# Kernel tuning notes

Measured on AMD Instinct MI355X. Metric: run time of the kernel, lower is better.

Reference implementation:

```python
import jax, jax.numpy as jnp
import numpy as np

B, S, D, H = 2, 2048, 1024, 16
DEPTH = D // H


def setup_inputs() -> dict:
    key = jax.random.key(0)
    ks = jax.random.split(key, 13)
    std = 1.0 / np.sqrt(D)
    inp = {
        'q': jax.random.normal(ks[0], (B, S, D), jnp.float32),
        'k': jax.random.normal(ks[1], (B, S, D), jnp.float32),
        'v': jax.random.normal(ks[2], (B, S, D), jnp.float32),
        # padding-style mask broadcastable to [B,H,Sq,Sk]; 1 = masked
        'mask': (jax.random.uniform(ks[3], (B, 1, 1, S)) < 0.1).astype(jnp.float32),
        'wq_w': jax.random.uniform(ks[4], (D, D), jnp.float32, -std, std),
        'wq_b': jax.random.uniform(ks[5], (D,), jnp.float32, -std, std),
        'wk_w': jax.random.uniform(ks[6], (D, D), jnp.float32, -std, std),
        'wk_b': jax.random.uniform(ks[7], (D,), jnp.float32, -std, std),
        'wv_w': jax.random.uniform(ks[8], (D, D), jnp.float32, -std, std),
        'wv_b': jax.random.uniform(ks[9], (D,), jnp.float32, -std, std),
        'wo_w': jax.random.uniform(ks[10], (D, D), jnp.float32, -std, std),
        'wo_b': jax.random.uniform(ks[11], (D,), jnp.float32, -std, std),
    }
    return inp


def _split_heads(x):
    # [B,S,D] -> [B,H,S,depth]
    b, s, _ = x.shape
    return x.reshape(b, s, H, DEPTH).transpose(0, 2, 1, 3)


def reference(q, k, v, mask, wq_w, wq_b, wk_w, wk_b, wv_w, wv_b, wo_w, wo_b):
    qh = _split_heads(q @ wq_w.T + wq_b)
    kh = _split_heads(k @ wk_w.T + wk_b)
    vh = _split_heads(v @ wv_w.T + wv_b)
    scale = 1.0 / jnp.sqrt(jnp.float32(DEPTH))
    logits = jnp.einsum('bhqd,bhkd->bhqk', qh, kh) * scale  # [B,H,S,S]
    logits = logits + mask * (-1e9)
    weights = jax.nn.softmax(logits, axis=-1)
    attn = jnp.einsum('bhqk,bhkd->bhqd', weights, vh)
    concat = attn.transpose(0, 2, 1, 3).reshape(q.shape[0], -1, D)
    out = concat @ wo_w.T + wo_b
    return out, weights
```

## Files before the change

### kernel.cpp

```cpp
#include <hip/hip_runtime.h>
#include <stdint.h>
#include <stddef.h>

static constexpr int NB = 2;
static constexpr int SS = 2048;
static constexpr int DDim = 1024;
static constexpr int NH = 16;
static constexpr size_t BSD = (size_t)NB * SS * DDim;
static constexpr size_t DDn = (size_t)DDim * DDim;

typedef __attribute__((ext_vector_type(4))) float f32x4;
typedef __attribute__((ext_vector_type(8))) short bf16x8;

__device__ __forceinline__ short f2bf(float f) {
  union { float f; unsigned u; } v; v.f = f;
  unsigned r = v.u + 0x7FFFu + ((v.u >> 16) & 1u);
  return (short)(r >> 16);
}

__device__ __forceinline__ void gload_lds16(const void* src, void* dst) {
  __builtin_amdgcn_global_load_lds(
      (const __attribute__((address_space(1))) void*)src,
      (__attribute__((address_space(3))) void*)dst, 16, 0, 0);
}

__global__ void cvt_k(const float* __restrict__ in, short* __restrict__ out, int n8) {
  int i = blockIdx.x * 256 + threadIdx.x;
  if (i >= n8) return;
  const f32x4* p = (const f32x4*)in + (size_t)i * 2;
  f32x4 a = p[0], c = p[1];
  bf16x8 o;
  o[0] = f2bf(a[0]); o[1] = f2bf(a[1]); o[2] = f2bf(a[2]); o[3] = f2bf(a[3]);
  o[4] = f2bf(c[0]); o[5] = f2bf(c[1]); o[6] = f2bf(c[2]); o[7] = f2bf(c[3]);
  ((bf16x8*)out)[i] = o;
}

__device__ __forceinline__ void gemm_core(
    const short* __restrict__ A, const short* __restrict__ Bm,
    int rowA, int rowB, int ld, int nk,
    short* la, short* lb, int wid, int lane, f32x4 (&acc)[4][4]) {
  const int ar = lane & 15, ak = (lane >> 4) * 8;
  const int srow = lane >> 2, scol = (lane & 3) * 8;
  const int wr = wid >> 1, wc = wid & 1;
  for (int kt = 0; kt < nk; ++kt) {
    const int k0 = kt * 32;
#pragma unroll
    for (int c = 0; c < 2; ++c) {
      int chunk = c * 4 + wid;
      gload_lds16(A + (size_t)(rowA + chunk * 16 + srow) * ld + k0 + scol, la + chunk * 512);
      gload_lds16(Bm + (size_t)(rowB + chunk * 16 + srow) * ld + k0 + scol, lb + chunk * 512);
    }
    asm volatile("s_waitcnt vmcnt(0)" ::: "memory");
    __syncthreads();
    bf16x8 af[4], bfr[4];
#pragma unroll
    for (int m = 0; m < 4; ++m)
      af[m] = *(const bf16x8*)(la + (wr * 64 + m * 16 + ar) * 32 + ak);
#pragma unroll
    for (int n = 0; n < 4; ++n)
      bfr[n] = *(const bf16x8*)(lb + (wc * 64 + n * 16 + ar) * 32 + ak);
#pragma unroll
    for (int m = 0; m < 4; ++m)
#pragma unroll
      for (int n = 0; n < 4; ++n)
        acc[m][n] = __builtin_amdgcn_mfma_f32_16x16x32_bf16(af[m], bfr[n], acc[m][n], 0, 0, 0);
    __syncthreads();
  }
}

template <int MODE>
__global__ __launch_bounds__(256, 2) void gemm128(
    const short* __restrict__ A, const short* __restrict__ Bm,
    const float* __restrict__ bias, void* __restrict__ outp, int N, int ld, int nk) {
  __shared__ short la[128 * 32], lb[128 * 32];
  const int tid = threadIdx.x, wid = tid >> 6, lane = tid & 63;
  const int bM = blockIdx.y * 128, bN = blockIdx.x * 128;
  f32x4 acc[4][4];
#pragma unroll
  for (int m = 0; m < 4; ++m)
#pragma unroll
    for (int n = 0; n < 4; ++n) acc[m][n] = (f32x4){0.f, 0.f, 0.f, 0.f};
  gemm_core(A, Bm, bM, bN, ld, nk, la, lb, wid, lane, acc);
  const int wr = wid >> 1, wc = wid & 1;
#pragma unroll
  for (int m = 0; m < 4; ++m)
#pragma unroll
    for (int n = 0; n < 4; ++n)
#pragma unroll
      for (int r = 0; r < 4; ++r) {
        int gm = bM + wr * 64 + m * 16 + (lane >> 4) * 4 + r;
        int gn = bN + wc * 64 + n * 16 + (lane & 15);
        float val = acc[m][n][r] + bias[gn];
        if constexpr (MODE == 0) {
          int b = gm >> 11, s = gm & 2047, h = gn >> 6, d = gn & 63;
          ((short*)outp)[(((size_t)b * NH + h) * SS + s) * 64 + d] = f2bf(val);
        } else if constexpr (MODE == 1) {
          int b = gm >> 11, s = gm & 2047, h = gn >> 6, d = gn & 63;
          ((short*)outp)[(((size_t)b * NH + h) * 64 + d) * SS + s] = f2bf(val);
        } else {
          ((float*)outp)[(size_t)gm * N + gn] = val;
        }
      }
}

__global__ __launch_bounds__(256, 2) void attn_k(
    const short* __restrict__ qh, const short* __restrict__ kh,
    const short* __restrict__ vhT, const float* __restrict__ mask,
    float* __restrict__ wout, short* __restrict__ concat) {
  __shared__ short lP[128 * 128];
  __shared__ short lK[128 * 64];
  __shared__ short lV[64 * 128];
  __shared__ float lmask[2048];
  __shared__ float lrs[2][128];
  const int tid = threadIdx.x, wid = tid >> 6, lane = tid & 63;
  const int wr = wid >> 1, wc = wid & 1;
  const int bh = blockIdx.y, b = bh >> 4, h = bh & 15;
  const int bM = blockIdx.x * 128;
  const short* Qb = qh + (size_t)bh * SS * 64 + (size_t)bM * 64;
  const short* Kb = kh + (size_t)bh * SS * 64;
  const short* Vb = vhT + (size_t)bh * 64 * SS;
  float* Wb = wout + (size_t)bh * SS * SS;

#pragma unroll
  for (int i = 0; i < 8; ++i)
    lmask[tid + i * 256] = mask[b * SS + tid + i * 256] * (-1e9f);

#pragma unroll
  for (int c = 0; c < 4; ++c) {
    int ob = c * 4096 + tid * 16;
    int row = ob >> 7, inrow = ob & 127;
    gload_lds16(Qb + row * 64 + ((inrow ^ ((row & 7) << 4)) >> 1), (char*)lP + ob);
  }
  asm volatile("s_waitcnt vmcnt(0)" ::: "memory");
  __syncthreads();
  bf16x8 af[4][2];
#pragma unroll
  for (int m = 0; m < 4; ++m)
#pragma unroll
    for (int kk = 0; kk < 2; ++kk) {
      int row = wr * 64 + m * 16 + (lane & 15);
      int kb = (kk * 32 + (lane >> 4) * 8) * 2;
      af[m][kk] = *(const bf16x8*)((const char*)lP + row * 128 + (kb ^ ((row & 7) << 4)));
    }

  float ps[4][4];
#pragma unroll
  for (int m = 0; m < 4; ++m)
#pragma unroll
    for (int r = 0; r < 4; ++r) ps[m][r] = 0.f;

  for (int kt = 0; kt < 16; ++kt) {
    __syncthreads();
#pragma unroll
    for (int c = 0; c < 4; ++c) {
      int ob = c * 4096 + tid * 16;
      int row = ob >> 7, inrow = ob & 127;
      gload_lds16(Kb + (size_t)(kt * 128 + row) * 64 + ((inrow ^ ((row & 7) << 4)) >> 1),
                  (char*)lK + ob);
    }
    asm volatile("s_waitcnt vmcnt(0)" ::: "memory");
    __syncthreads();
    bf16x8 bfr[4][2];
#pragma unroll
    for (int n = 0; n < 4; ++n)
#pragma unroll
      for (int kk = 0; kk < 2; ++kk) {
        int row = wc * 64 + n * 16 + (lane & 15);
        int kb = (kk * 32 + (lane >> 4) * 8) * 2;
        bfr[n][kk] = *(const bf16x8*)((const char*)lK + row * 128 + (kb ^ ((row & 7) << 4)));
      }
#pragma unroll
    for (int n = 0; n < 4; ++n) {
      float mv = lmask[kt * 128 + wc * 64 + n * 16 + (lane & 15)];
#pragma unroll
      for (int m = 0; m < 4; ++m) {
        f32x4 a = (f32x4){0.f, 0.f, 0.f, 0.f};
        a = __builtin_amdgcn_mfma_f32_16x16x32_bf16(af[m][0], bfr[n][0], a, 0, 0, 0);
        a = __builtin_amdgcn_mfma_f32_16x16x32_bf16(af[m][1], bfr[n][1], a, 0, 0, 0);
#pragma unroll
        for (int r = 0; r < 4; ++r) ps[m][r] += __expf(a[r] * 0.125f + mv);
      }
    }
  }
#pragma unroll
  for (int m = 0; m < 4; ++m)
#pragma unroll
    for (int r = 0; r < 4; ++r) {
      float s = ps[m][r];
      s += __shfl_xor(s, 1, 64);
      s += __shfl_xor(s, 2, 64);
      s += __shfl_xor(s, 4, 64);
      s += __shfl_xor(s, 8, 64);
      ps[m][r] = s;
    }
  if ((lane & 15) == 0) {
#pragma unroll
    for (int m = 0; m < 4; ++m)
#pragma unroll
      for (int r = 0; r < 4; ++r)
        lrs[wc][wr * 64 + m * 16 + (lane >> 4) * 4 + r] = ps[m][r];
  }
  __syncthreads();
  float inv[4][4];
#pragma unroll
  for (int m = 0; m < 4; ++m)
#pragma unroll
    for (int r = 0; r < 4; ++r) {
      int row = wr * 64 + m * 16 + (lane >> 4) * 4 + r;
      inv[m][r] = 1.f / (lrs[0][row] + lrs[1][row]);
    }

  f32x4 pacc[4][2];
#pragma unroll
  for (int m = 0; m < 4; ++m)
#pragma unroll
    for (int n = 0; n < 2; ++n) pacc[m][n] = (f32x4){0.f, 0.f, 0.f, 0.f};

  for (int kt = 0; kt < 16; ++kt) {
    __syncthreads();
#pragma unroll
    for (int c = 0; c < 4; ++c) {
      int ob = c * 4096 + tid * 16;
      int row = ob >> 7, inrow = ob & 127;
      gload_lds16(Kb + (size_t)(kt * 128 + row) * 64 + ((inrow ^ ((row & 7) << 4)) >> 1),
                  (char*)lK + ob);
    }
#pragma unroll
    for (int c = 0; c < 4; ++c) {
      int ob = c * 4096 + tid * 16;
      int row = ob >> 8, inrow = ob & 255;
      gload_lds16(Vb + (size_t)row * SS + kt * 128 + ((inrow ^ ((row & 7) << 4)) >> 1),
                  (char*)lV + ob);
    }
    asm volatile("s_waitcnt vmcnt(0)" ::: "memory");
    __syncthreads();
    bf16x8 bfr[4][2];
#pragma unroll
    for (int n = 0; n < 4; ++n)
#pragma unroll
      for (int kk = 0; kk < 2; ++kk) {
        int row = wc * 64 + n * 16 + (lane & 15);
        int kb = (kk * 32 + (lane >> 4) * 8) * 2;
        bfr[n][kk] = *(const bf16x8*)((const char*)lK + row * 128 + (kb ^ ((row & 7) << 4)));
      }
#pragma unroll
    for (int n = 0; n < 4; ++n) {
      int col = wc * 64 + n * 16 + (lane & 15);
      float mv = lmask[kt * 128 + col];
#pragma unroll
      for (int m = 0; m < 4; ++m) {
        f32x4 a = (f32x4){0.f, 0.f, 0.f, 0.f};
        a = __builtin_amdgcn_mfma_f32_16x16x32_bf16(af[m][0], bfr[n][0], a, 0, 0, 0);
        a = __builtin_amdgcn_mfma_f32_16x16x32_bf16(af[m][1], bfr[n][1], a, 0, 0, 0);
#pragma unroll
        for (int r = 0; r < 4; ++r) {
          int prow = wr * 64 + m * 16 + (lane >> 4) * 4 + r;
          float w = __expf(a[r] * 0.125f + mv) * inv[m][r];
          Wb[(size_t)(bM + prow) * SS + kt * 128 + col] = w;
          *(short*)((char*)lP + prow * 256 + ((col * 2) ^ ((prow & 7) << 4))) = f2bf(w);
        }
      }
    }
    __syncthreads();
#pragma unroll
    for (int kk = 0; kk < 4; ++kk) {
      bf16x8 pa[4], bv[2];
      int kb = (kk * 32 + (lane >> 4) * 8) * 2;
#pragma unroll
      for (int m = 0; m < 4; ++m) {
        int row = wr * 64 + m * 16 + (lane & 15);
        pa[m] = *(const bf16x8*)((const char*)lP + row * 256 + (kb ^ ((row & 7) << 4)));
      }
#pragma unroll
      for (int n = 0; n < 2; ++n) {
        int d = wc * 32 + n * 16 + (lane & 15);
        bv[n] = *(const bf16x8*)((const char*)lV + d * 256 + (kb ^ ((d & 7) << 4)));
      }
#pragma unroll
      for (int m = 0; m < 4; ++m)
#pragma unroll
        for (int n = 0; n < 2; ++n)
          pacc[m][n] = __builtin_amdgcn_mfma_f32_16x16x32_bf16(pa[m], bv[n], pacc[m][n], 0, 0, 0);
    }
  }
#pragma unroll
  for (int m = 0; m < 4; ++m)
#pragma unroll
    for (int n = 0; n < 2; ++n)
#pragma unroll
      for (int r = 0; r < 4; ++r) {
        int s = bM + wr * 64 + m * 16 + (lane >> 4) * 4 + r;
        int d = wc * 32 + n * 16 + (lane & 15);
        concat[((size_t)(b * SS + s)) * DDim + h * 64 + d] = f2bf(pacc[m][n][r]);
      }
}

extern "C" void kernel_launch(void* const* d_in, const int* in_sizes, int n_in,
                              void* d_out, int out_size, void* d_ws, size_t ws_size,
                              hipStream_t stream) {
  const float* q = (const float*)d_in[0];
  const float* k = (const float*)d_in[1];
  const float* v = (const float*)d_in[2];
  const float* mask = (const float*)d_in[3];
  const float* wq_w = (const float*)d_in[4];
  const float* wq_b = (const float*)d_in[5];
  const float* wk_w = (const float*)d_in[6];
  const float* wk_b = (const float*)d_in[7];
  const float* wv_w = (const float*)d_in[8];
  const float* wv_b = (const float*)d_in[9];
  const float* wo_w = (const float*)d_in[10];
  const float* wo_b = (const float*)d_in[11];

  short* qb = (short*)d_ws;
  short* kb = qb + BSD;
  short* vb = kb + BSD;
  short* wqb = vb + BSD;
  short* wkb = wqb + DDn;
  short* wvb = wkb + DDn;
  short* wob = wvb + DDn;
  short* qh = wob + DDn;
  short* kh = qh + BSD;
  short* vhT = kh + BSD;
  short* concat = vhT + BSD;

  float* out0 = (float*)d_out;
  float* wts = out0 + BSD;

  const int n8_bsd = (int)(BSD / 8), n8_dd = (int)(DDn / 8);
  cvt_k<<<n8_bsd / 256, 256, 0, stream>>>(q, qb, n8_bsd);
  cvt_k<<<n8_bsd / 256, 256, 0, stream>>>(k, kb, n8_bsd);
  cvt_k<<<n8_bsd / 256, 256, 0, stream>>>(v, vb, n8_bsd);
  cvt_k<<<n8_dd / 256, 256, 0, stream>>>(wq_w, wqb, n8_dd);
  cvt_k<<<n8_dd / 256, 256, 0, stream>>>(wk_w, wkb, n8_dd);
  cvt_k<<<n8_dd / 256, 256, 0, stream>>>(wv_w, wvb, n8_dd);
  cvt_k<<<n8_dd / 256, 256, 0, stream>>>(wo_w, wob, n8_dd);

  dim3 gproj(DDim / 128, (NB * SS) / 128);
  gemm128<0><<<gproj, 256, 0, stream>>>(qb, wqb, wq_b, qh, DDim, DDim, DDim / 32);
  gemm128<0><<<gproj, 256, 0, stream>>>(kb, wkb, wk_b, kh, DDim, DDim, DDim / 32);
  gemm128<1><<<gproj, 256, 0, stream>>>(vb, wvb, wv_b, vhT, DDim, DDim, DDim / 32);

  dim3 gattn(SS / 128, NB * NH);
  attn_k<<<gattn, 256, 0, stream>>>(qh, kh, vhT, mask, wts, concat);

  gemm128<2><<<gproj, 256, 0, stream>>>(concat, wob, wo_b, (void*)out0, DDim, DDim, DDim / 32);
}
```

Baseline: 331.4 us.

## Double-buffer GEMM and attention K/V tiles, enlarge attention block to 256 rows

Measured after the change: 375.6 us. +13.4%, slower.

```diff
diff --git a/kernel.cpp b/kernel.cpp
--- a/kernel.cpp
+++ b/kernel.cpp
@@ -11,6 +11,9 @@
 
 typedef __attribute__((ext_vector_type(4))) float f32x4;
 typedef __attribute__((ext_vector_type(8))) short bf16x8;
+
+static constexpr float SCL2 = 0.125f * 1.4426950408889634f;
+static constexpr float MSK2 = -1.4426950408889634e9f;
 
 __device__ __forceinline__ short f2bf(float f) {
   union { float f; unsigned u; } v; v.f = f;
@@ -35,53 +38,53 @@
   ((bf16x8*)out)[i] = o;
 }
 
-__device__ __forceinline__ void gemm_core(
-    const short* __restrict__ A, const short* __restrict__ Bm,
-    int rowA, int rowB, int ld, int nk,
-    short* la, short* lb, int wid, int lane, f32x4 (&acc)[4][4]) {
-  const int ar = lane & 15, ak = (lane >> 4) * 8;
-  const int srow = lane >> 2, scol = (lane & 3) * 8;
-  const int wr = wid >> 1, wc = wid & 1;
-  for (int kt = 0; kt < nk; ++kt) {
-    const int k0 = kt * 32;
-#pragma unroll
-    for (int c = 0; c < 2; ++c) {
-      int chunk = c * 4 + wid;
-      gload_lds16(A + (size_t)(rowA + chunk * 16 + srow) * ld + k0 + scol, la + chunk * 512);
-      gload_lds16(Bm + (size_t)(rowB + chunk * 16 + srow) * ld + k0 + scol, lb + chunk * 512);
-    }
-    asm volatile("s_waitcnt vmcnt(0)" ::: "memory");
-    __syncthreads();
-    bf16x8 af[4], bfr[4];
-#pragma unroll
-    for (int m = 0; m < 4; ++m)
-      af[m] = *(const bf16x8*)(la + (wr * 64 + m * 16 + ar) * 32 + ak);
-#pragma unroll
-    for (int n = 0; n < 4; ++n)
-      bfr[n] = *(const bf16x8*)(lb + (wc * 64 + n * 16 + ar) * 32 + ak);
-#pragma unroll
-    for (int m = 0; m < 4; ++m)
-#pragma unroll
-      for (int n = 0; n < 4; ++n)
-        acc[m][n] = __builtin_amdgcn_mfma_f32_16x16x32_bf16(af[m], bfr[n], acc[m][n], 0, 0, 0);
-    __syncthreads();
-  }
-}
-
 template <int MODE>
 __global__ __launch_bounds__(256, 2) void gemm128(
     const short* __restrict__ A, const short* __restrict__ Bm,
     const float* __restrict__ bias, void* __restrict__ outp, int N, int ld, int nk) {
-  __shared__ short la[128 * 32], lb[128 * 32];
+  __shared__ short la[2][4096], lb[2][4096];
   const int tid = threadIdx.x, wid = tid >> 6, lane = tid & 63;
   const int bM = blockIdx.y * 128, bN = blockIdx.x * 128;
+  const int ar = lane & 15, ak = (lane >> 4) * 8;
+  const int srow = lane >> 2, scol = (lane & 3) * 8;
+  const int wr = wid >> 1, wc = wid & 1;
   f32x4 acc[4][4];
 #pragma unroll
   for (int m = 0; m < 4; ++m)
 #pragma unroll
     for (int n = 0; n < 4; ++n) acc[m][n] = (f32x4){0.f, 0.f, 0.f, 0.f};
-  gemm_core(A, Bm, bM, bN, ld, nk, la, lb, wid, lane, acc);
-  const int wr = wid >> 1, wc = wid & 1;
+
+  auto stage = [&](int kt, int bb) {
+    const int k0 = kt * 32;
+#pragma unroll
+    for (int c = 0; c < 2; ++c) {
+      int chunk = c * 4 + wid;
+      gload_lds16(A + (size_t)(bM + chunk * 16 + srow) * ld + k0 + scol, &la[bb][chunk * 512]);
+      gload_lds16(Bm + (size_t)(bN + chunk * 16 + srow) * ld + k0 + scol, &lb[bb][chunk * 512]);
+    }
+  };
+
+  stage(0, 0);
+  asm volatile("s_waitcnt vmcnt(0)" ::: "memory");
+  __syncthreads();
+  for (int kt = 0; kt < nk; ++kt) {
+    const int bb = kt & 1;
+    if (kt + 1 < nk) stage(kt + 1, bb ^ 1);
+    bf16x8 af[4], bfr[4];
+#pragma unroll
+    for (int m = 0; m < 4; ++m)
+      af[m] = *(const bf16x8*)(&la[bb][(wr * 64 + m * 16 + ar) * 32 + ak]);
+#pragma unroll
+    for (int n = 0; n < 4; ++n)
+      bfr[n] = *(const bf16x8*)(&lb[bb][(wc * 64 + n * 16 + ar) * 32 + ak]);
+#pragma unroll
+    for (int m = 0; m < 4; ++m)
+#pragma unroll
+      for (int n = 0; n < 4; ++n)
+        acc[m][n] = __builtin_amdgcn_mfma_f32_16x16x32_bf16(af[m], bfr[n], acc[m][n], 0, 0, 0);
+    asm volatile("s_waitcnt vmcnt(0)" ::: "memory");
+    __syncthreads();
+  }
 #pragma unroll
   for (int m = 0; m < 4; ++m)
 #pragma unroll
@@ -103,34 +106,54 @@
       }
 }
 
-__global__ __launch_bounds__(256, 2) void attn_k(
+__global__ __launch_bounds__(512, 2) void attn_k(
     const short* __restrict__ qh, const short* __restrict__ kh,
     const short* __restrict__ vhT, const float* __restrict__ mask,
     float* __restrict__ wout, short* __restrict__ concat) {
-  __shared__ short lP[128 * 128];
-  __shared__ short lK[128 * 64];
-  __shared__ short lV[64 * 128];
+  __shared__ short lP[256 * 128];
+  __shared__ short lK[2][128 * 64];
+  __shared__ short lV[2][64 * 128];
   __shared__ float lmask[2048];
-  __shared__ float lrs[2][128];
+  __shared__ float lrs[2][256];
   const int tid = threadIdx.x, wid = tid >> 6, lane = tid & 63;
   const int wr = wid >> 1, wc = wid & 1;
-  const int bh = blockIdx.y, b = bh >> 4, h = bh & 15;
-  const int bM = blockIdx.x * 128;
+  const int bh = blockIdx.x, b = bh >> 4, h = bh & 15;
+  const int bM = blockIdx.y * 256;
   const short* Qb = qh + (size_t)bh * SS * 64 + (size_t)bM * 64;
   const short* Kb = kh + (size_t)bh * SS * 64;
   const short* Vb = vhT + (size_t)bh * 64 * SS;
   float* Wb = wout + (size_t)bh * SS * SS;
 
 #pragma unroll
-  for (int i = 0; i < 8; ++i)
-    lmask[tid + i * 256] = mask[b * SS + tid + i * 256] * (-1e9f);
+  for (int i = 0; i < 4; ++i)
+    lmask[tid + i * 512] = mask[b * SS + tid + i * 512] * MSK2;
+
+  auto stageK = [&](int kt, int bb) {
+#pragma unroll
+    for (int c = 0; c < 2; ++c) {
+      int ob = c * 8192 + tid * 16;
+      int row = ob >> 7, inrow = ob & 127;
+      gload_lds16(Kb + (size_t)(kt * 128 + row) * 64 + ((inrow ^ ((row & 7) << 4)) >> 1),
+                  (char*)lK[bb] + ob);
+    }
+  };
+  auto stageV = [&](int kt, int bb) {
+#pragma unroll
+    for (int c = 0; c < 2; ++c) {
+      int ob = c * 8192 + tid * 16;
+      int row = ob >> 8, inrow = ob & 255;
+      gload_lds16(Vb + (size_t)row * SS + kt * 128 + ((inrow ^ ((row & 7) << 4)) >> 1),
+                  (char*)lV[bb] + ob);
+    }
+  };
 
 #pragma unroll
   for (int c = 0; c < 4; ++c) {
-    int ob = c * 4096 + tid * 16;
+    int ob = c * 8192 + tid * 16;
     int row = ob >> 7, inrow = ob & 127;
     gload_lds16(Qb + row * 64 + ((inrow ^ ((row & 7) << 4)) >> 1), (char*)lP + ob);
   }
+  stageK(0, 0);
   asm volatile("s_waitcnt vmcnt(0)" ::: "memory");
   __syncthreads();
   bf16x8 af[4][2];
@@ -142,6 +165,7 @@
       int kb = (kk * 32 + (lane >> 4) * 8) * 2;
       af[m][kk] = *(const bf16x8*)((const char*)lP + row * 128 + (kb ^ ((row & 7) << 4)));
     }
+  __syncthreads();
 
   float ps[4][4];
 #pragma unroll
@@ -150,16 +174,8 @@
     for (int r = 0; r < 4; ++r) ps[m][r] = 0.f;
 
   for (int kt = 0; kt < 16; ++kt) {
-    __syncthreads();
-#pragma unroll
-    for (int c = 0; c < 4; ++c) {
-      int ob = c * 4096 + tid * 16;
-      int row = ob >> 7, inrow = ob & 127;
-      gload_lds16(Kb + (size_t)(kt * 128 + row) * 64 + ((inrow ^ ((row & 7) << 4)) >> 1),
-                  (char*)lK + ob);
-    }
-    asm volatile("s_waitcnt vmcnt(0)" ::: "memory");
-    __syncthreads();
+    const int bb = kt & 1;
+    if (kt < 15) stageK(kt + 1, bb ^ 1);
     bf16x8 bfr[4][2];
 #pragma unroll
     for (int n = 0; n < 4; ++n)
@@ -167,7 +183,7 @@
       for (int kk = 0; kk < 2; ++kk) {
         int row = wc * 64 + n * 16 + (lane & 15);
         int kb = (kk * 32 + (lane >> 4) * 8) * 2;
-        bfr[n][kk] = *(const bf16x8*)((const char*)lK + row * 128 + (kb ^ ((row & 7) << 4)));
+        bfr[n][kk] = *(const bf16x8*)((const char*)lK[bb] + row * 128 + (kb ^ ((row & 7) << 4)));
       }
 #pragma unroll
     for (int n = 0; n < 4; ++n) {
@@ -178,9 +194,11 @@
         a = __builtin_amdgcn_mfma_f32_16x16x32_bf16(af[m][0], bfr[n][0], a, 0, 0, 0);
         a = __builtin_amdgcn_mfma_f32_16x16x32_bf16(af[m][1], bfr[n][1], a, 0, 0, 0);
 #pragma unroll
-        for (int r = 0; r < 4; ++r) ps[m][r] += __expf(a[r] * 0.125f + mv);
-      }
-    }
+        for (int r = 0; r < 4; ++r) ps[m][r] += exp2f(a[r] * SCL2 + mv);
+      }
+    }
+    asm volatile("s_waitcnt vmcnt(0)" ::: "memory");
+    __syncthreads();
   }
 #pragma unroll
   for (int m = 0; m < 4; ++m)
@@ -200,6 +218,8 @@
       for (int r = 0; r < 4; ++r)
         lrs[wc][wr * 64 + m * 16 + (lane >> 4) * 4 + r] = ps[m][r];
   }
+  stageK(0, 0);
+  stageV(0, 0);
   __syncthreads();
   float inv[4][4];
 #pragma unroll
@@ -209,6 +229,8 @@
       int row = wr * 64 + m * 16 + (lane >> 4) * 4 + r;
       inv[m][r] = 1.f / (lrs[0][row] + lrs[1][row]);
     }
+  asm volatile("s_waitcnt vmcnt(0)" ::: "memory");
+  __syncthreads();
 
   f32x4 pacc[4][2];
 #pragma unroll
@@ -217,23 +239,7 @@
     for (int n = 0; n < 2; ++n) pacc[m][n] = (f32x4){0.f, 0.f, 0.f, 0.f};
 
   for (int kt = 0; kt < 16; ++kt) {
-    __syncthreads();
-#pragma unroll
-    for (int c = 0; c < 4; ++c) {
-      int ob = c * 4096 + tid * 16;
-      int row = ob >> 7, inrow = ob & 127;
-      gload_lds16(Kb + (size_t)(kt * 128 + row) * 64 + ((inrow ^ ((row & 7) << 4)) >> 1),
-                  (char*)lK + ob);
-    }
-#pragma unroll
-    for (int c = 0; c < 4; ++c) {
-      int ob = c * 4096 + tid * 16;
-      int row = ob >> 8, inrow = ob & 255;
-      gload_lds16(Vb + (size_t)row * SS + kt * 128 + ((inrow ^ ((row & 7) << 4)) >> 1),
-                  (char*)lV + ob);
-    }
-    asm volatile("s_waitcnt vmcnt(0)" ::: "memory");
-    __syncthreads();
+    const int bb = kt & 1;
     bf16x8 bfr[4][2];
 #pragma unroll
     for (int n = 0; n < 4; ++n)
@@ -241,8 +247,12 @@
       for (int kk = 0; kk < 2; ++kk) {
         int row = wc * 64 + n * 16 + (lane & 15);
         int kb = (kk * 32 + (lane >> 4) * 8) * 2;
-        bfr[n][kk] = *(const bf16x8*)((const char*)lK + row * 128 + (kb ^ ((row & 7) << 4)));
-      }
+        bfr[n][kk] = *(const bf16x8*)((const char*)lK[bb] + row * 128 + (kb ^ ((row & 7) << 4)));
+      }
+    if (kt < 15) {
+      stageK(kt + 1, bb ^ 1);
+      stageV(kt + 1, bb ^ 1);
+    }
 #pragma unroll
     for (int n = 0; n < 4; ++n) {
       int col = wc * 64 + n * 16 + (lane & 15);
@@ -255,7 +265,7 @@
 #pragma unroll
         for (int r = 0; r < 4; ++r) {
           int prow = wr * 64 + m * 16 + (lane >> 4) * 4 + r;
-          float w = __expf(a[r] * 0.125f + mv) * inv[m][r];
+          float w = exp2f(a[r] * SCL2 + mv) * inv[m][r];
           Wb[(size_t)(bM + prow) * SS + kt * 128 + col] = w;
           *(short*)((char*)lP + prow * 256 + ((col * 2) ^ ((prow & 7) << 4))) = f2bf(w);
         }
@@ -274,7 +284,7 @@
 #pragma unroll
       for (int n = 0; n < 2; ++n) {
         int d = wc * 32 + n * 16 + (lane & 15);
-        bv[n] = *(const bf16x8*)((const char*)lV + d * 256 + (kb ^ ((d & 7) << 4)));
+        bv[n] = *(const bf16x8*)((const char*)lV[bb] + d * 256 + (kb ^ ((d & 7) << 4)));
       }
 #pragma unroll
       for (int m = 0; m < 4; ++m)
@@ -282,6 +292,8 @@
         for (int n = 0; n < 2; ++n)
           pacc[m][n] = __builtin_amdgcn_mfma_f32_16x16x32_bf16(pa[m], bv[n], pacc[m][n], 0, 0, 0);
     }
+    asm volatile("s_waitcnt vmcnt(0)" ::: "memory");
+    __syncthreads();
   }
 #pragma unroll
   for (int m = 0; m < 4; ++m)
@@ -340,8 +352,8 @@
   gemm128<0><<<gproj, 256, 0, stream>>>(kb, wkb, wk_b, kh, DDim, DDim, DDim / 32);
   gemm128<1><<<gproj, 256, 0, stream>>>(vb, wvb, wv_b, vhT, DDim, DDim, DDim / 32);
 
-  dim3 gattn(SS / 128, NB * NH);
-  attn_k<<<gattn, 256, 0, stream>>>(qh, kh, vhT, mask, wts, concat);
+  dim3 gattn(NB * NH, SS / 256);
+  attn_k<<<gattn, 512, 0, stream>>>(qh, kh, vhT, mask, wts, concat);
 
   gemm128<2><<<gproj, 256, 0, stream>>>(concat, wob, wo_b, (void*)out0, DDim, DDim, DDim / 32);
 }
```
